# Performance work log

Measured on AMD Instinct MI355X. Metric: run time of the kernel, lower is better.

Reference implementation:

```python
import jax, jax.numpy as jnp
import numpy as np

EPS = 1e-5
NUM_GROUPS = 32


def setup_inputs() -> dict:
    key = jax.random.key(0)
    B, C, H, W = 16, 512, 32, 32
    ks = jax.random.split(key, 5)
    s = 1.0 / np.sqrt(C)  # keep attention logits well-scaled
    return {
        "x": jax.random.normal(ks[0], (B, C, H, W), jnp.float32),
        "gamma": jnp.ones((C,), jnp.float32),
        "beta": jnp.zeros((C,), jnp.float32),
        "wq": jax.random.normal(ks[1], (C, C), jnp.float32) * s,
        "bq": jnp.zeros((C,), jnp.float32),
        "wk": jax.random.normal(ks[2], (C, C), jnp.float32) * s,
        "bk": jnp.zeros((C,), jnp.float32),
        "wv": jax.random.normal(ks[3], (C, C), jnp.float32) * s,
        "bv": jnp.zeros((C,), jnp.float32),
        "wp": jax.random.normal(ks[4], (C, C), jnp.float32) * s,
        "bp": jnp.zeros((C,), jnp.float32),
    }


def _group_norm(x, gamma, beta):
    B, C, H, W = x.shape
    g = NUM_GROUPS
    xg = x.reshape(B, g, C // g, H * W)
    mu = jnp.mean(xg, axis=(2, 3), keepdims=True)
    var = jnp.mean(jnp.square(xg - mu), axis=(2, 3), keepdims=True)
    h = (xg - mu) * jax.lax.rsqrt(var + EPS)
    h = h.reshape(B, C, H, W)
    return h * gamma[None, :, None, None] + beta[None, :, None, None]


def reference(x, gamma, beta, wq, bq, wk, bk, wv, bv, wp, bp):
    B, C, H, W = x.shape
    N = H * W
    h = _group_norm(x, gamma, beta).reshape(B, C, N)  # [B,C,N]
    # 1x1 convs == per-pixel matmuls over channels
    q = jnp.einsum('oc,bcn->bon', wq, h) + bq[None, :, None]
    k = jnp.einsum('oc,bcn->bon', wk, h) + bk[None, :, None]
    v = jnp.einsum('oc,bcn->bon', wv, h) + bv[None, :, None]
    scale = int(C) ** (-0.5)
    logits = jnp.einsum('bcn,bcm->bnm', q, k) * scale  # [B,N,N]
    attn = jax.nn.softmax(logits, axis=-1)
    o = jnp.einsum('bnm,bcm->bcn', attn, v)  # [B,C,N]
    out = jnp.einsum('oc,bcn->bon', wp, o) + bp[None, :, None]
    return x + out.reshape(B, C, H, W)
```

## Files before the change

### kernel.cpp

```cpp
#include <hip/hip_runtime.h>
#include <hip/hip_bf16.h>

typedef __attribute__((ext_vector_type(8))) short bf16x8;
typedef __attribute__((ext_vector_type(4))) float f32x4;
typedef __attribute__((ext_vector_type(8))) unsigned short u16x8;
typedef __attribute__((ext_vector_type(4))) unsigned short u16x4;

static __device__ __forceinline__ unsigned short f2bf(float f) {
  __hip_bfloat16 h = __float2bfloat16(f);
  union { __hip_bfloat16 h; unsigned short u; } cv; cv.h = h; return cv.u;
}
static __device__ __forceinline__ float bf2f(unsigned short u) {
  union { unsigned int u; float f; } cv; cv.u = ((unsigned int)u) << 16; return cv.f;
}

static __device__ __forceinline__ void gload16(const unsigned short* g, unsigned short* l) {
  __builtin_amdgcn_global_load_lds((const __attribute__((address_space(1))) void*)g,
                                   (__attribute__((address_space(3))) void*)l, 16, 0, 0);
}

#define BK 32
#define EPW 134

__global__ __launch_bounds__(256, 2) void gemm_bt(
    const unsigned short* __restrict__ A, const unsigned short* __restrict__ Bm,
    long sA, long sB, int lda, int ldb, int K,
    const float* __restrict__ bias, int bias_mode, float post_scale,
    int out_mode, void* __restrict__ D, long sD, int ldd,
    const float* __restrict__ resid)
{
  extern __shared__ unsigned short smem[];
  const int gx = gridDim.x, gy = gridDim.y;
  const int nwg = gx * gy * gridDim.z;
  int orig = blockIdx.x + gx * (blockIdx.y + gy * blockIdx.z);
  int id = (orig & 7) * (nwg >> 3) + (orig >> 3);
  const int bxi = id % gx;
  int rem = id / gx;
  const int byi = rem % gy;
  const int bz = rem / gy;

  const int tid = threadIdx.x, lane = tid & 63, wid = tid >> 6;
  const int l15 = lane & 15, lhi = lane >> 4;
  const int wr = wid >> 1, wc = wid & 1;
  const long bm = (long)byi * 128, bn = (long)bxi * 128;
  const unsigned short* Ab = A + (size_t)bz * sA + (size_t)bm * lda;
  const unsigned short* Bb = Bm + (size_t)bz * sB + (size_t)bn * ldb;
  const int NT = K >> 5;

  f32x4 acc[4][4];
  #pragma unroll
  for (int i = 0; i < 4; ++i)
    #pragma unroll
    for (int j = 0; j < 4; ++j) acc[i][j] = (f32x4){0.f, 0.f, 0.f, 0.f};

  auto stage = [&](int t) {
    const int slot = t & 3;
    const int k0 = t * BK;
    #pragma unroll
    for (int j = 0; j < 2; ++j) {
      int bi = j * 256 + tid;
      int row = bi >> 2, sl = bi & 3;
      int kb = sl ^ ((row >> 1) & 3);
      gload16(Ab + (size_t)row * lda + k0 + kb * 8,
              &smem[slot * 8192 + (j * 256 + wid * 64) * 8]);
    }
    #pragma unroll
    for (int j = 0; j < 2; ++j) {
      int bi = j * 256 + tid;
      int row = bi >> 2, sl = bi & 3;
      int kb = sl ^ ((row >> 1) & 3);
      gload16(Bb + (size_t)row * ldb + k0 + kb * 8,
              &smem[slot * 8192 + 4096 + (j * 256 + wid * 64) * 8]);
    }
  };

  stage(0); stage(1); stage(2);

  for (int t = 0; t < NT; ++t) {
    const int ahead = NT - 1 - t;
    if (ahead >= 2)      asm volatile("s_waitcnt vmcnt(8)" ::: "memory");
    else if (ahead == 1) asm volatile("s_waitcnt vmcnt(4)" ::: "memory");
    else                 asm volatile("s_waitcnt vmcnt(0)" ::: "memory");
    asm volatile("s_waitcnt lgkmcnt(0)" ::: "memory");
    __builtin_amdgcn_s_barrier();
    asm volatile("" ::: "memory");

    const int slot = t & 3;
    bf16x8 af[4], bfr[4];
    #pragma unroll
    for (int mi = 0; mi < 4; ++mi) {
      int row = wr * 64 + mi * 16 + l15;
      int sl = lhi ^ ((row >> 1) & 3);
      af[mi] = *(const bf16x8*)&smem[slot * 8192 + row * BK + sl * 8];
    }
    #pragma unroll
    for (int ni = 0; ni < 4; ++ni) {
      int row = wc * 64 + ni * 16 + l15;
      int sl = lhi ^ ((row >> 1) & 3);
      bfr[ni] = *(const bf16x8*)&smem[slot * 8192 + 4096 + row * BK + sl * 8];
    }
    if (t + 3 < NT) stage(t + 3);
    #pragma unroll
    for (int mi = 0; mi < 4; ++mi)
      #pragma unroll
      for (int ni = 0; ni < 4; ++ni)
        acc[mi][ni] = __builtin_amdgcn_mfma_f32_16x16x32_bf16(af[mi], bfr[ni], acc[mi][ni], 0, 0, 0);
  }
  __syncthreads();

  if (out_mode == 0) {
    #pragma unroll
    for (int mi = 0; mi < 4; ++mi) {
      #pragma unroll
      for (int ni = 0; ni < 4; ++ni) {
        #pragma unroll
        for (int r = 0; r < 4; ++r) {
          int rl = wr * 64 + mi * 16 + lhi * 4 + r;
          int cl = wc * 64 + ni * 16 + l15;
          float v = acc[mi][ni][r];
          if (bias_mode == 1) v += bias[bm + rl];
          else if (bias_mode == 2) v += bias[bn + cl];
          v *= post_scale;
          smem[rl * EPW + cl] = f2bf(v);
        }
      }
    }
    __syncthreads();
    const int row = tid >> 1, hf = tid & 1;
    unsigned short* dst = (unsigned short*)D + (size_t)bz * sD + (size_t)(bm + row) * ldd + bn + hf * 64;
    const unsigned short* src = &smem[row * EPW + hf * 64];
    #pragma unroll
    for (int j = 0; j < 8; ++j) *(u16x8*)&dst[j * 8] = *(const u16x8*)&src[j * 8];
  } else {
    float* smf = (float*)smem;
    float* outF = (float*)D;
    #pragma unroll
    for (int h = 0; h < 2; ++h) {
      if (wr == h) {
        #pragma unroll
        for (int mi = 0; mi < 4; ++mi)
          #pragma unroll
          for (int ni = 0; ni < 4; ++ni)
            #pragma unroll
            for (int r = 0; r < 4; ++r) {
              int rl = mi * 16 + lhi * 4 + r;
              int cl = wc * 64 + ni * 16 + l15;
              float v = acc[mi][ni][r];
              if (bias_mode == 1) v += bias[bm + h * 64 + rl];
              smf[rl * EPW + cl] = v * post_scale;
            }
      }
      __syncthreads();
      const int rl = tid >> 2, q = tid & 3;
      const long rowg = bm + h * 64 + rl;
      #pragma unroll
      for (int j = 0; j < 8; ++j) {
        long col = bn + q * 32 + j * 4;
        long b = col >> 10, n = col & 1023;
        size_t oi = (size_t)b * 524288 + (size_t)rowg * 1024 + n;
        float4 v = *(const float4*)&smf[rl * EPW + q * 32 + j * 4];
        float4 xr = *(const float4*)&resid[oi];
        float4 o = { v.x + xr.x, v.y + xr.y, v.z + xr.z, v.w + xr.w };
        *(float4*)&outF[oi] = o;
      }
      __syncthreads();
    }
  }
}

__global__ __launch_bounds__(256) void groupnorm_to_ht(
    const float* __restrict__ x, const float* __restrict__ gamma,
    const float* __restrict__ beta, unsigned short* __restrict__ ht)
{
  const int b = blockIdx.x >> 5;
  const int g = blockIdx.x & 31;
  const int tid = threadIdx.x, lane = tid & 63, wid = tid >> 6;
  const float4* xg4 = (const float4*)(x + ((size_t)b * 512 + g * 16) * 1024);
  float4 v[16];
  float s = 0.f, ss = 0.f;
  #pragma unroll
  for (int j = 0; j < 16; ++j) {
    v[j] = xg4[j * 256 + tid];
    s += v[j].x + v[j].y + v[j].z + v[j].w;
    ss += v[j].x * v[j].x + v[j].y * v[j].y + v[j].z * v[j].z + v[j].w * v[j].w;
  }
  #pragma unroll
  for (int o = 32; o; o >>= 1) { s += __shfl_xor(s, o); ss += __shfl_xor(ss, o); }
  __shared__ float red[8];
  if (lane == 0) { red[wid] = s; red[4 + wid] = ss; }
  __syncthreads();
  s = red[0] + red[1] + red[2] + red[3];
  ss = red[4] + red[5] + red[6] + red[7];
  const float mu = s * (1.f / 16384.f);
  const float var = ss * (1.f / 16384.f) - mu * mu;
  const float rsig = rsqrtf(var + 1e-5f);
  __shared__ unsigned short tile[16][1024];
  #pragma unroll
  for (int j = 0; j < 16; ++j) {
    int e = (j * 256 + tid) * 4;
    int ci = e >> 10, n = e & 1023;
    float ga = gamma[g * 16 + ci] * rsig, be = beta[g * 16 + ci];
    u16x4 o = { f2bf((v[j].x - mu) * ga + be), f2bf((v[j].y - mu) * ga + be),
                f2bf((v[j].z - mu) * ga + be), f2bf((v[j].w - mu) * ga + be) };
    *(u16x4*)&tile[ci][n] = o;
  }
  __syncthreads();
  unsigned short* hb = ht + (size_t)b * 1024 * 512 + g * 16;
  for (int rep = 0; rep < 4; ++rep) {
    int n = rep * 256 + tid;
    u16x8 lo, hi;
    #pragma unroll
    for (int ci = 0; ci < 8; ++ci) lo[ci] = tile[ci][n];
    #pragma unroll
    for (int ci = 0; ci < 8; ++ci) hi[ci] = tile[8 + ci][n];
    *(u16x8*)&hb[(size_t)n * 512] = lo;
    *(u16x8*)&hb[(size_t)n * 512 + 8] = hi;
  }
}

__global__ __launch_bounds__(256) void softmax_rows(unsigned short* __restrict__ attn)
{
  int row = blockIdx.x * 4 + (threadIdx.x >> 6);
  int lane = threadIdx.x & 63;
  unsigned short* p = attn + (size_t)row * 1024;
  u16x8 c0 = *(const u16x8*)&p[lane * 8];
  u16x8 c1 = *(const u16x8*)&p[512 + lane * 8];
  float f[16];
  #pragma unroll
  for (int j = 0; j < 8; ++j) { f[j] = bf2f(c0[j]); f[8 + j] = bf2f(c1[j]); }
  float m = f[0];
  #pragma unroll
  for (int j = 1; j < 16; ++j) m = fmaxf(m, f[j]);
  #pragma unroll
  for (int o = 32; o; o >>= 1) m = fmaxf(m, __shfl_xor(m, o));
  float sum = 0.f;
  #pragma unroll
  for (int j = 0; j < 16; ++j) { f[j] = __expf(f[j] - m); sum += f[j]; }
  #pragma unroll
  for (int o = 32; o; o >>= 1) sum += __shfl_xor(sum, o);
  float inv = 1.0f / sum;
  #pragma unroll
  for (int j = 0; j < 8; ++j) { c0[j] = f2bf(f[j] * inv); c1[j] = f2bf(f[8 + j] * inv); }
  *(u16x8*)&p[lane * 8] = c0;
  *(u16x8*)&p[512 + lane * 8] = c1;
}

__global__ __launch_bounds__(256) void convert_weights(
    const float* __restrict__ wq, const float* __restrict__ wk,
    const float* __restrict__ wv, const float* __restrict__ wp,
    const float* __restrict__ bq, const float* __restrict__ bk,
    unsigned short* __restrict__ out, float* __restrict__ bqk)
{
  if (blockIdx.x == 1024) {
    int i = threadIdx.x * 4;
    if (i < 512) *(float4*)&bqk[i] = *(const float4*)&bq[i];
    else         *(float4*)&bqk[i] = *(const float4*)&bk[i - 512];
    return;
  }
  int t = blockIdx.x * 256 + threadIdx.x;
  int m = t >> 16;
  int off = (t & 65535) * 4;
  const float* src = m == 0 ? wq : m == 1 ? wk : m == 2 ? wv : wp;
  float4 v = *(const float4*)&src[off];
  u16x4 o = { f2bf(v.x), f2bf(v.y), f2bf(v.z), f2bf(v.w) };
  *(u16x4*)&out[(size_t)m * 262144 + off] = o;
}

extern "C" void kernel_launch(void* const* d_in, const int* in_sizes, int n_in,
                              void* d_out, int out_size, void* d_ws, size_t ws_size,
                              hipStream_t stream)
{
  const float* x     = (const float*)d_in[0];
  const float* gamma = (const float*)d_in[1];
  const float* beta  = (const float*)d_in[2];
  const float* wq    = (const float*)d_in[3];
  const float* bq    = (const float*)d_in[4];
  const float* wk    = (const float*)d_in[5];
  const float* bk    = (const float*)d_in[6];
  const float* wv    = (const float*)d_in[7];
  const float* bv    = (const float*)d_in[8];
  const float* wp    = (const float*)d_in[9];
  const float* bp    = (const float*)d_in[10];

  unsigned short* ws   = (unsigned short*)d_ws;
  unsigned short* w_bf = ws;
  unsigned short* ht   = w_bf + 1048576;
  unsigned short* qk   = ht + 8388608;
  unsigned short* vv2  = qk + 16777216;
  unsigned short* attn = vv2 + 8388608;
  unsigned short* ot   = attn + 16777216;
  float*          bqk  = (float*)(ot + 8388608);

  const float scale = 0.044194173824159216f;
  const int SMEM = 65536;
  hipFuncSetAttribute(reinterpret_cast<const void*>(&gemm_bt),
                      hipFuncAttributeMaxDynamicSharedMemorySize, SMEM);

  convert_weights<<<dim3(1025), dim3(256), 0, stream>>>(wq, wk, wv, wp, bq, bk, w_bf, bqk);
  groupnorm_to_ht<<<dim3(512), dim3(256), 0, stream>>>(x, gamma, beta, ht);

  gemm_bt<<<dim3(8, 128, 1), dim3(256), SMEM, stream>>>(
      ht, w_bf, 0L, 0L, 512, 512, 512,
      bqk, 2, 1.0f, 0, (void*)qk, 0L, 1024, (const float*)nullptr);
  gemm_bt<<<dim3(128, 4, 1), dim3(256), SMEM, stream>>>(
      w_bf + 2 * 262144, ht, 0L, 0L, 512, 512, 512,
      bv, 1, 1.0f, 0, (void*)vv2, 0L, 16384, (const float*)nullptr);
  gemm_bt<<<dim3(8, 8, 16), dim3(256), SMEM, stream>>>(
      qk, qk + 512, 1048576L, 1048576L, 1024, 1024, 512,
      (const float*)nullptr, 0, scale, 0, (void*)attn, 1048576L, 1024, (const float*)nullptr);
  softmax_rows<<<dim3(4096), dim3(256), 0, stream>>>(attn);
  gemm_bt<<<dim3(4, 8, 16), dim3(256), SMEM, stream>>>(
      attn, vv2, 1048576L, 1024L, 1024, 16384, 1024,
      (const float*)nullptr, 0, 1.0f, 0, (void*)ot, 524288L, 512, (const float*)nullptr);
  gemm_bt<<<dim3(128, 4, 1), dim3(256), SMEM, stream>>>(
      w_bf + 3 * 262144, ot, 0L, 0L, 512, 512, 512,
      bp, 1, 1.0f, 1, d_out, 0L, 16384, x);
}
```

Before: 206.1 us.

## Enlarge GEMM tiles to 256x128 with 512 threads and double-buffered LDS

The batched bf16 GEMM moves from a 128x128 tile with 256 threads and a 4-stage global_load_lds pipeline to a 256x128 tile with 8 waves and a 2-buffer static LDS scheme that synchronises once per K step. The epilogues are rewritten to stage half or a quarter of the tile at a time through the smaller LDS, and the grids are halved to match. The aim is more operand reuse per block and less launch/grid overhead. In exchange, the shallower prefetch exposes more global-load latency, since each iteration issues the next stage and then computes with no explicit vmcnt wait. The launch bound of 4 blocks of 512 threads also limits registers per thread.

```diff
diff --git a/kernel.cpp b/kernel.cpp
--- a/kernel.cpp
+++ b/kernel.cpp
@@ -19,17 +19,21 @@
                                    (__attribute__((address_space(3))) void*)l, 16, 0, 0);
 }
 
+#define BM 256
+#define BN 128
 #define BK 32
-#define EPW 134
-
-__global__ __launch_bounds__(256, 2) void gemm_bt(
+
+__global__ __launch_bounds__(512, 4) void gemm_bt(
     const unsigned short* __restrict__ A, const unsigned short* __restrict__ Bm,
     long sA, long sB, int lda, int ldb, int K,
     const float* __restrict__ bias, int bias_mode, float post_scale,
     int out_mode, void* __restrict__ D, long sD, int ldd,
     const float* __restrict__ resid)
 {
-  extern __shared__ unsigned short smem[];
+  __shared__ __align__(16) unsigned char smem_raw[49152];
+  unsigned short* lA = (unsigned short*)smem_raw;
+  unsigned short* lB = (unsigned short*)(smem_raw + 32768);
+
   const int gx = gridDim.x, gy = gridDim.y;
   const int nwg = gx * gy * gridDim.z;
   int orig = blockIdx.x + gx * (blockIdx.y + gy * blockIdx.z);
@@ -42,7 +46,7 @@
   const int tid = threadIdx.x, lane = tid & 63, wid = tid >> 6;
   const int l15 = lane & 15, lhi = lane >> 4;
   const int wr = wid >> 1, wc = wid & 1;
-  const long bm = (long)byi * 128, bn = (long)bxi * 128;
+  const long bm = (long)byi * BM, bn = (long)bxi * BN;
   const unsigned short* Ab = A + (size_t)bz * sA + (size_t)bm * lda;
   const unsigned short* Bb = Bm + (size_t)bz * sB + (size_t)bn * ldb;
   const int NT = K >> 5;
@@ -53,90 +57,87 @@
     #pragma unroll
     for (int j = 0; j < 4; ++j) acc[i][j] = (f32x4){0.f, 0.f, 0.f, 0.f};
 
-  auto stage = [&](int t) {
-    const int slot = t & 3;
-    const int k0 = t * BK;
+  auto stage = [&](int buf, int k0) {
     #pragma unroll
     for (int j = 0; j < 2; ++j) {
-      int bi = j * 256 + tid;
+      int bi = j * 512 + tid;
       int row = bi >> 2, sl = bi & 3;
       int kb = sl ^ ((row >> 1) & 3);
       gload16(Ab + (size_t)row * lda + k0 + kb * 8,
-              &smem[slot * 8192 + (j * 256 + wid * 64) * 8]);
-    }
-    #pragma unroll
-    for (int j = 0; j < 2; ++j) {
-      int bi = j * 256 + tid;
-      int row = bi >> 2, sl = bi & 3;
+              lA + buf * 8192 + (j * 512 + wid * 64) * 8);
+    }
+    {
+      int row = tid >> 2, sl = tid & 3;
       int kb = sl ^ ((row >> 1) & 3);
       gload16(Bb + (size_t)row * ldb + k0 + kb * 8,
-              &smem[slot * 8192 + 4096 + (j * 256 + wid * 64) * 8]);
+              lB + buf * 4096 + wid * 512);
     }
   };
 
-  stage(0); stage(1); stage(2);
-
+  stage(0, 0);
+  __syncthreads();
+  int buf = 0;
   for (int t = 0; t < NT; ++t) {
-    const int ahead = NT - 1 - t;
-    if (ahead >= 2)      asm volatile("s_waitcnt vmcnt(8)" ::: "memory");
-    else if (ahead == 1) asm volatile("s_waitcnt vmcnt(4)" ::: "memory");
-    else                 asm volatile("s_waitcnt vmcnt(0)" ::: "memory");
-    asm volatile("s_waitcnt lgkmcnt(0)" ::: "memory");
-    __builtin_amdgcn_s_barrier();
-    asm volatile("" ::: "memory");
-
-    const int slot = t & 3;
+    if (t + 1 < NT) stage(buf ^ 1, (t + 1) * BK);
     bf16x8 af[4], bfr[4];
     #pragma unroll
     for (int mi = 0; mi < 4; ++mi) {
       int row = wr * 64 + mi * 16 + l15;
       int sl = lhi ^ ((row >> 1) & 3);
-      af[mi] = *(const bf16x8*)&smem[slot * 8192 + row * BK + sl * 8];
+      af[mi] = *(const bf16x8*)&lA[buf * 8192 + row * 32 + sl * 8];
     }
     #pragma unroll
     for (int ni = 0; ni < 4; ++ni) {
       int row = wc * 64 + ni * 16 + l15;
       int sl = lhi ^ ((row >> 1) & 3);
-      bfr[ni] = *(const bf16x8*)&smem[slot * 8192 + 4096 + row * BK + sl * 8];
-    }
-    if (t + 3 < NT) stage(t + 3);
+      bfr[ni] = *(const bf16x8*)&lB[buf * 4096 + row * 32 + sl * 8];
+    }
     #pragma unroll
     for (int mi = 0; mi < 4; ++mi)
       #pragma unroll
       for (int ni = 0; ni < 4; ++ni)
         acc[mi][ni] = __builtin_amdgcn_mfma_f32_16x16x32_bf16(af[mi], bfr[ni], acc[mi][ni], 0, 0, 0);
-  }
-  __syncthreads();
+    __syncthreads();
+    buf ^= 1;
+  }
 
   if (out_mode == 0) {
-    #pragma unroll
-    for (int mi = 0; mi < 4; ++mi) {
+    unsigned short* ep = (unsigned short*)smem_raw;
+    #pragma unroll
+    for (int h = 0; h < 2; ++h) {
+      if ((wr >> 1) == h) {
+        #pragma unroll
+        for (int mi = 0; mi < 4; ++mi)
+          #pragma unroll
+          for (int ni = 0; ni < 4; ++ni)
+            #pragma unroll
+            for (int r = 0; r < 4; ++r) {
+              int rl = (wr & 1) * 64 + mi * 16 + lhi * 4 + r;
+              int cl = wc * 64 + ni * 16 + l15;
+              float v = acc[mi][ni][r];
+              if (bias_mode == 1) v += bias[bm + h * 128 + rl];
+              else if (bias_mode == 2) v += bias[bn + cl];
+              ep[rl * 136 + cl] = f2bf(v * post_scale);
+            }
+      }
+      __syncthreads();
       #pragma unroll
-      for (int ni = 0; ni < 4; ++ni) {
-        #pragma unroll
-        for (int r = 0; r < 4; ++r) {
-          int rl = wr * 64 + mi * 16 + lhi * 4 + r;
-          int cl = wc * 64 + ni * 16 + l15;
-          float v = acc[mi][ni][r];
-          if (bias_mode == 1) v += bias[bm + rl];
-          else if (bias_mode == 2) v += bias[bn + cl];
-          v *= post_scale;
-          smem[rl * EPW + cl] = f2bf(v);
-        }
+      for (int i = 0; i < 4; ++i) {
+        int c = i * 512 + tid;
+        int row = c >> 4, pos = c & 15;
+        unsigned short* dst = (unsigned short*)D + (size_t)bz * sD
+                            + (size_t)(bm + h * 128 + row) * ldd + bn + pos * 8;
+        *(u16x8*)dst = *(const u16x8*)&ep[row * 136 + pos * 8];
       }
-    }
-    __syncthreads();
-    const int row = tid >> 1, hf = tid & 1;
-    unsigned short* dst = (unsigned short*)D + (size_t)bz * sD + (size_t)(bm + row) * ldd + bn + hf * 64;
-    const unsigned short* src = &smem[row * EPW + hf * 64];
-    #pragma unroll
-    for (int j = 0; j < 8; ++j) *(u16x8*)&dst[j * 8] = *(const u16x8*)&src[j * 8];
+      __syncthreads();
+    }
   } else {
-    float* smf = (float*)smem;
+    float* epf = (float*)smem_raw;
     float* outF = (float*)D;
-    #pragma unroll
-    for (int h = 0; h < 2; ++h) {
-      if (wr == h) {
+    const long bq_ = bn >> 10, n0 = bn & 1023;
+    #pragma unroll
+    for (int qd = 0; qd < 4; ++qd) {
+      if (wr == qd) {
         #pragma unroll
         for (int mi = 0; mi < 4; ++mi)
           #pragma unroll
@@ -146,19 +147,17 @@
               int rl = mi * 16 + lhi * 4 + r;
               int cl = wc * 64 + ni * 16 + l15;
               float v = acc[mi][ni][r];
-              if (bias_mode == 1) v += bias[bm + h * 64 + rl];
-              smf[rl * EPW + cl] = v * post_scale;
+              if (bias_mode == 1) v += bias[bm + qd * 64 + rl];
+              epf[rl * 132 + cl] = v * post_scale;
             }
       }
       __syncthreads();
-      const int rl = tid >> 2, q = tid & 3;
-      const long rowg = bm + h * 64 + rl;
       #pragma unroll
-      for (int j = 0; j < 8; ++j) {
-        long col = bn + q * 32 + j * 4;
-        long b = col >> 10, n = col & 1023;
-        size_t oi = (size_t)b * 524288 + (size_t)rowg * 1024 + n;
-        float4 v = *(const float4*)&smf[rl * EPW + q * 32 + j * 4];
+      for (int i = 0; i < 4; ++i) {
+        int c = i * 512 + tid;
+        int row = c >> 5, pos = c & 31;
+        size_t oi = (size_t)bq_ * 524288 + (size_t)(bm + qd * 64 + row) * 1024 + n0 + pos * 4;
+        float4 v = *(const float4*)&epf[row * 132 + pos * 4];
         float4 xr = *(const float4*)&resid[oi];
         float4 o = { v.x + xr.x, v.y + xr.y, v.z + xr.z, v.w + xr.w };
         *(float4*)&outF[oi] = o;
@@ -292,27 +291,24 @@
   float*          bqk  = (float*)(ot + 8388608);
 
   const float scale = 0.044194173824159216f;
-  const int SMEM = 65536;
-  hipFuncSetAttribute(reinterpret_cast<const void*>(&gemm_bt),
-                      hipFuncAttributeMaxDynamicSharedMemorySize, SMEM);
 
   convert_weights<<<dim3(1025), dim3(256), 0, stream>>>(wq, wk, wv, wp, bq, bk, w_bf, bqk);
   groupnorm_to_ht<<<dim3(512), dim3(256), 0, stream>>>(x, gamma, beta, ht);
 
-  gemm_bt<<<dim3(8, 128, 1), dim3(256), SMEM, stream>>>(
+  gemm_bt<<<dim3(8, 64, 1), dim3(512), 0, stream>>>(
       ht, w_bf, 0L, 0L, 512, 512, 512,
       bqk, 2, 1.0f, 0, (void*)qk, 0L, 1024, (const float*)nullptr);
-  gemm_bt<<<dim3(128, 4, 1), dim3(256), SMEM, stream>>>(
+  gemm_bt<<<dim3(128, 2, 1), dim3(512), 0, stream>>>(
       w_bf + 2 * 262144, ht, 0L, 0L, 512, 512, 512,
       bv, 1, 1.0f, 0, (void*)vv2, 0L, 16384, (const float*)nullptr);
-  gemm_bt<<<dim3(8, 8, 16), dim3(256), SMEM, stream>>>(
+  gemm_bt<<<dim3(8, 4, 16), dim3(512), 0, stream>>>(
       qk, qk + 512, 1048576L, 1048576L, 1024, 1024, 512,
       (const float*)nullptr, 0, scale, 0, (void*)attn, 1048576L, 1024, (const float*)nullptr);
   softmax_rows<<<dim3(4096), dim3(256), 0, stream>>>(attn);
-  gemm_bt<<<dim3(4, 8, 16), dim3(256), SMEM, stream>>>(
+  gemm_bt<<<dim3(4, 4, 16), dim3(512), 0, stream>>>(
       attn, vv2, 1048576L, 1024L, 1024, 16384, 1024,
       (const float*)nullptr, 0, 1.0f, 0, (void*)ot, 524288L, 512, (const float*)nullptr);
-  gemm_bt<<<dim3(128, 4, 1), dim3(256), SMEM, stream>>>(
+  gemm_bt<<<dim3(128, 2, 1), dim3(512), 0, stream>>>(
       w_bf + 3 * 262144, ot, 0L, 0L, 512, 512, 512,
       bp, 1, 1.0f, 1, d_out, 0L, 16384, x);
 }
```

Result: faster. 191.0 us (-7.3%).
